# Optimization experiments

Measured on AMD Instinct MI355X. Metric: run time of the kernel, lower is better.

## Reference

```python
import jax, jax.numpy as jnp
import numpy as np

B, N, D, H, S = 32, 8192, 64, 128, 16
ITERS, TAU = 3, 0.1


def _ln(x, g, b):
    m = x.mean(-1, keepdims=True)
    v = ((x - m) ** 2).mean(-1, keepdims=True)
    return (x - m) / jnp.sqrt(v + 1e-5) * g + b


def setup_inputs() -> dict:
    key = jax.random.key(0)
    ks = jax.random.split(key, 20)
    nrm = lambda k, shp, s: jax.random.normal(k, shp, jnp.float32) * s
    return {
        'x': nrm(ks[0], (B, N, D), 1.0),
        'w1': nrm(ks[1], (D, H), D ** -0.5), 'b1': jnp.zeros((H,), jnp.float32),
        'ln1_g': jnp.ones((H,), jnp.float32), 'ln1_b': jnp.zeros((H,), jnp.float32),
        'w2': nrm(ks[2], (H, H), H ** -0.5), 'b2': jnp.zeros((H,), jnp.float32),
        'ln2_g': jnp.ones((H,), jnp.float32), 'ln2_b': jnp.zeros((H,), jnp.float32),
        'slot_mu': nrm(ks[3], (1, S, H), 0.1),
        'gru_wi': nrm(ks[4], (3 * H, H), H ** -0.5), 'gru_wh': nrm(ks[5], (3 * H, H), H ** -0.5),
        'gru_bi': jnp.zeros((3 * H,), jnp.float32), 'gru_bh': jnp.zeros((3 * H,), jnp.float32),
        'mlp_w1': nrm(ks[6], (H, H), H ** -0.5), 'mlp_b1': jnp.zeros((H,), jnp.float32),
        'mlp_w2': nrm(ks[7], (H, H), H ** -0.5), 'mlp_b2': jnp.zeros((H,), jnp.float32),
        'norm_g': jnp.ones((H,), jnp.float32), 'norm_b': jnp.zeros((H,), jnp.float32),
    }


def reference(x, w1, b1, ln1_g, ln1_b, w2, b2, ln2_g, ln2_b, slot_mu,
              gru_wi, gru_wh, gru_bi, gru_bh, mlp_w1, mlp_b1, mlp_w2, mlp_b2,
              norm_g, norm_b):
    Bb = x.shape[0]
    h = jax.nn.gelu(_ln(x @ w1 + b1, ln1_g, ln1_b), approximate=False)
    feats = _ln(h @ w2 + b2, ln2_g, ln2_b)              # [B,N,H]
    slots = jnp.broadcast_to(slot_mu, (Bb, S, H))
    f2 = jnp.sum(feats * feats, -1)                      # [B,N]
    attn = None
    for _ in range(ITERS):
        s2 = jnp.sum(slots * slots, -1)                  # [B,S]
        sf = jnp.einsum('bsh,bnh->bsn', slots, feats)
        dist_sq = -(s2[:, :, None] - 2.0 * sf + f2[:, None, :])  # -||s-f||^2
        attn = jax.nn.softmax(dist_sq / TAU, axis=1)     # softmax over slots
        w = attn / (attn.sum(2, keepdims=True) + 1e-8)
        updates = jnp.einsum('bsn,bnh->bsh', w, feats)
        # GRUCell (PyTorch gate order: r, z, n)
        gi = updates @ gru_wi.T + gru_bi
        gh = slots @ gru_wh.T + gru_bh
        ir, iz, inn = jnp.split(gi, 3, -1)
        hr, hz, hn = jnp.split(gh, 3, -1)
        r = jax.nn.sigmoid(ir + hr)
        z = jax.nn.sigmoid(iz + hz)
        n = jnp.tanh(inn + r * hn)
        new = (1.0 - z) * n + z * slots
        mlp_out = jax.nn.gelu(_ln(new, norm_g, norm_b) @ mlp_w1 + mlp_b1, approximate=False) @ mlp_w2 + mlp_b2
        slots = new + 0.2 * mlp_out
    return (slots, attn)
```

## Files before the change

kernel.cpp:

```cpp
#include <hip/hip_runtime.h>
#include <cstddef>
#include <cstdint>

#define B_ 32
#define N_ 8192
#define D_ 64
#define H_ 128
#define S_ 16
#define L2SCALE 14.426950408889634f

typedef unsigned short ushort_t;
typedef __attribute__((ext_vector_type(8))) short short8;
typedef __attribute__((ext_vector_type(4))) float f32x4;

#define NCHUNK 256
#define NBLK   (N_ / NCHUNK)
#define PSTRIDE 264

#define W1T_STR 72
#define W2T_STR 136

__device__ __forceinline__ float gelu_fast(float x){
    float z = fabsf(x) * 0.70710678118654752f;
    float t = 1.0f / fmaf(0.3275911f, z, 1.0f);
    float p = t*(0.254829592f + t*(-0.284496736f + t*(1.421413741f +
              t*(-1.453152027f + t*1.061405429f))));
    float e = __expf(-z*z);
    float erf_abs = 1.0f - p*e;
    float er = copysignf(erf_abs, x);
    return 0.5f * x * (1.0f + er);
}
__device__ __forceinline__ ushort_t f2bf(float f){
    unsigned u = __float_as_uint(f);
    unsigned r = (u + 0x7FFF + ((u >> 16) & 1)) >> 16;
    return (ushort_t)r;
}
__device__ __forceinline__ float bf2f(ushort_t h){
    return __uint_as_float(((unsigned)h) << 16);
}

__global__ __launch_bounds__(256) void gemm1_kernel(
    const float* __restrict__ x, const float* __restrict__ w1, const float* __restrict__ b1,
    const float* __restrict__ ln1g, const float* __restrict__ ln1b,
    ushort_t* __restrict__ h_hi, ushort_t* __restrict__ h_lo)
{
    __shared__ ushort_t w1t_hi[128*W1T_STR];
    __shared__ ushort_t w1t_lo[128*W1T_STR];

    const int tid  = threadIdx.x;
    const int w    = tid >> 6;
    const int l    = tid & 63;
    const int ln   = l & 15;
    const int quad = l >> 4;
    const size_t n0 = (size_t)blockIdx.x * 128;

    for (int i = tid; i < 8192; i += 256){
        int k = i >> 7, hc = i & 127;
        float v = w1[i];
        ushort_t hi = f2bf(v);
        w1t_hi[hc*W1T_STR + k] = hi;
        w1t_lo[hc*W1T_STR + k] = f2bf(v - bf2f(hi));
    }
    __syncthreads();

    for (int tt = 0; tt < 2; ++tt){
        const size_t row = n0 + (size_t)(w*2 + tt)*16 + ln;
        const float* xr = x + row*64;

        short8 bxh[2], bxl[2];
        #pragma unroll
        for (int kc = 0; kc < 2; ++kc){
            float4 a0 = *(const float4*)(xr + kc*32 + quad*8);
            float4 a1 = *(const float4*)(xr + kc*32 + quad*8 + 4);
            float v[8] = {a0.x,a0.y,a0.z,a0.w,a1.x,a1.y,a1.z,a1.w};
            #pragma unroll
            for (int j=0;j<8;++j){
                ushort_t hi = f2bf(v[j]);
                bxh[kc][j] = (short)hi;
                bxl[kc][j] = (short)f2bf(v[j] - bf2f(hi));
            }
        }

        f32x4 acc[8];
        #pragma unroll
        for (int ht=0;ht<8;++ht) acc[ht] = (f32x4){0.f,0.f,0.f,0.f};

        #pragma unroll
        for (int ht = 0; ht < 8; ++ht){
            #pragma unroll
            for (int kc = 0; kc < 2; ++kc){
                short8 ah = *(const short8*)&w1t_hi[(ht*16+ln)*W1T_STR + kc*32 + quad*8];
                short8 al = *(const short8*)&w1t_lo[(ht*16+ln)*W1T_STR + kc*32 + quad*8];
                acc[ht] = __builtin_amdgcn_mfma_f32_16x16x32_bf16(ah, bxh[kc], acc[ht], 0,0,0);
                acc[ht] = __builtin_amdgcn_mfma_f32_16x16x32_bf16(ah, bxl[kc], acc[ht], 0,0,0);
                acc[ht] = __builtin_amdgcn_mfma_f32_16x16x32_bf16(al, bxh[kc], acc[ht], 0,0,0);
            }
        }

        float vals[8][4];
        float s1 = 0.f, sq = 0.f;
        #pragma unroll
        for (int ht=0;ht<8;++ht){
            float bb[4]; *(float4*)bb = *(const float4*)(b1 + ht*16 + quad*4);
            #pragma unroll
            for (int r=0;r<4;++r){
                float v = acc[ht][r] + bb[r];
                vals[ht][r] = v; s1 += v; sq += v*v;
            }
        }
        s1 += __shfl_xor(s1,16); s1 += __shfl_xor(s1,32);
        sq += __shfl_xor(sq,16); sq += __shfl_xor(sq,32);
        float mean = s1 * (1.f/128.f);
        float var  = sq * (1.f/128.f) - mean*mean;
        float rs   = 1.f / sqrtf(var + 1e-5f);

        #pragma unroll
        for (int ht=0;ht<8;++ht){
            float gg[4]; *(float4*)gg = *(const float4*)(ln1g + ht*16 + quad*4);
            float be[4]; *(float4*)be = *(const float4*)(ln1b + ht*16 + quad*4);
            ushort_t oh[4], ol[4];
            #pragma unroll
            for (int r=0;r<4;++r){
                float t  = (vals[ht][r]-mean)*rs*gg[r] + be[r];
                float ge = gelu_fast(t);
                ushort_t hi = f2bf(ge);
                oh[r] = hi;
                ol[r] = f2bf(ge - bf2f(hi));
            }
            size_t off = row*128 + ht*16 + quad*4;
            *(ushort4*)(h_hi + off) = make_ushort4(oh[0],oh[1],oh[2],oh[3]);
            *(ushort4*)(h_lo + off) = make_ushort4(ol[0],ol[1],ol[2],ol[3]);
        }
    }
}

__global__ __launch_bounds__(256) void gemm2_kernel(
    ushort_t* __restrict__ buf_hi, ushort_t* __restrict__ buf_lo,
    const float* __restrict__ w2, const float* __restrict__ b2,
    const float* __restrict__ ln2g, const float* __restrict__ ln2b)
{
    __shared__ ushort_t w2t_hi[128*W2T_STR];
    __shared__ ushort_t w2t_lo[128*W2T_STR];

    const int tid  = threadIdx.x;
    const int w    = tid >> 6;
    const int l    = tid & 63;
    const int ln   = l & 15;
    const int quad = l >> 4;
    const size_t n0 = (size_t)blockIdx.x * 128;

    for (int i = tid; i < 16384; i += 256){
        int k = i >> 7, hc = i & 127;
        float v = w2[i];
        ushort_t hi = f2bf(v);
        w2t_hi[hc*W2T_STR + k] = hi;
        w2t_lo[hc*W2T_STR + k] = f2bf(v - bf2f(hi));
    }
    __syncthreads();

    size_t row[2];
    row[0] = n0 + (size_t)(w*2 + 0)*16 + ln;
    row[1] = n0 + (size_t)(w*2 + 1)*16 + ln;

    f32x4 acc[2][8];
    #pragma unroll
    for (int t2=0;t2<2;++t2)
        #pragma unroll
        for (int ht=0;ht<8;++ht) acc[t2][ht] = (f32x4){0.f,0.f,0.f,0.f};

    #pragma unroll
    for (int kc = 0; kc < 4; ++kc){
        short8 bh[2], bl[2];
        #pragma unroll
        for (int t2=0;t2<2;++t2){
            bh[t2] = *(const short8*)(buf_hi + row[t2]*128 + kc*32 + quad*8);
            bl[t2] = *(const short8*)(buf_lo + row[t2]*128 + kc*32 + quad*8);
        }
        #pragma unroll
        for (int ht = 0; ht < 8; ++ht){
            short8 ah = *(const short8*)&w2t_hi[(ht*16+ln)*W2T_STR + kc*32 + quad*8];
            short8 al = *(const short8*)&w2t_lo[(ht*16+ln)*W2T_STR + kc*32 + quad*8];
            #pragma unroll
            for (int t2=0;t2<2;++t2){
                acc[t2][ht] = __builtin_amdgcn_mfma_f32_16x16x32_bf16(ah, bh[t2], acc[t2][ht], 0,0,0);
                acc[t2][ht] = __builtin_amdgcn_mfma_f32_16x16x32_bf16(ah, bl[t2], acc[t2][ht], 0,0,0);
                acc[t2][ht] = __builtin_amdgcn_mfma_f32_16x16x32_bf16(al, bh[t2], acc[t2][ht], 0,0,0);
            }
        }
    }

    #pragma unroll
    for (int t2=0;t2<2;++t2){
        float vals[8][4];
        float s1 = 0.f, sq = 0.f;
        #pragma unroll
        for (int ht=0;ht<8;++ht){
            float bb[4]; *(float4*)bb = *(const float4*)(b2 + ht*16 + quad*4);
            #pragma unroll
            for (int r=0;r<4;++r){
                float v = acc[t2][ht][r] + bb[r];
                vals[ht][r] = v; s1 += v; sq += v*v;
            }
        }
        s1 += __shfl_xor(s1,16); s1 += __shfl_xor(s1,32);
        sq += __shfl_xor(sq,16); sq += __shfl_xor(sq,32);
        float mean = s1 * (1.f/128.f);
        float var  = sq * (1.f/128.f) - mean*mean;
        float rs   = 1.f / sqrtf(var + 1e-5f);
        #pragma unroll
        for (int ht=0;ht<8;++ht){
            float gg[4]; *(float4*)gg = *(const float4*)(ln2g + ht*16 + quad*4);
            float be[4]; *(float4*)be = *(const float4*)(ln2b + ht*16 + quad*4);
            ushort_t oh[4], ol[4];
            #pragma unroll
            for (int r=0;r<4;++r){
                float o = (vals[ht][r]-mean)*rs*gg[r] + be[r];
                ushort_t hi = f2bf(o);
                oh[r] = hi;
                ol[r] = f2bf(o - bf2f(hi));
            }
            size_t off = row[t2]*128 + ht*16 + quad*4;
            *(ushort4*)(buf_hi + off) = make_ushort4(oh[0],oh[1],oh[2],oh[3]);
            *(ushort4*)(buf_lo + off) = make_ushort4(ol[0],ol[1],ol[2],ol[3]);
        }
    }
}

__global__ void init_slots(const float* __restrict__ mu, float* __restrict__ slots){
    int i = blockIdx.x * 256 + threadIdx.x;
    slots[i] = mu[i & 2047];
}

__global__ __launch_bounds__(256, 3) void attn_kernel(
    const ushort_t* __restrict__ f_hi, const ushort_t* __restrict__ f_lo,
    const float* __restrict__ slots,
    float* __restrict__ pn, float* __restrict__ pd,
    float* __restrict__ attn_out, const int write_attn)
{
    __shared__ ushort_t P_hi[16*PSTRIDE];
    __shared__ ushort_t P_lo[16*PSTRIDE];
    __shared__ float    s2buf[16];
    __shared__ float    den_red[16];

    const int tid  = threadIdx.x;
    const int w    = tid >> 6;
    const int l    = tid & 63;
    const int ln   = l & 15;
    const int quad = l >> 4;
    const int b    = blockIdx.x >> 5;
    const int nc   = blockIdx.x & 31;
    const int n0   = nc * NCHUNK;

    if (tid < 16) den_red[tid] = 0.f;

    short8 sa_hi[4], sa_lo[4];
    float q2 = 0.f;
    {
        const float* sp = slots + ((size_t)(b*16 + ln))*128 + quad*8;
        #pragma unroll
        for (int ks=0; ks<4; ++ks){
            float4 v0 = *(const float4*)(sp + ks*32);
            float4 v1 = *(const float4*)(sp + ks*32 + 4);
            float v[8] = {v0.x,v0.y,v0.z,v0.w,v1.x,v1.y,v1.z,v1.w};
            #pragma unroll
            for (int j=0;j<8;++j){
                q2 += v[j]*v[j];
                ushort_t hi = f2bf(v[j]);
                float lo = v[j] - bf2f(hi);
                sa_hi[ks][j] = (short)hi;
                sa_lo[ks][j] = (short)f2bf(lo);
            }
        }
    }
    q2 += __shfl_xor(q2, 16);
    q2 += __shfl_xor(q2, 32);
    if (tid < 16) s2buf[tid] = q2;
    __syncthreads();

    float s2v[4];
    #pragma unroll
    for (int r=0;r<4;++r) s2v[r] = s2buf[quad*4 + r];

    float den_acc[4] = {0.f,0.f,0.f,0.f};
    const size_t fbase = (size_t)b*N_ + n0;

    #pragma unroll
    for (int t2=0; t2<4; ++t2){
        const int t  = w*4 + t2;
        const int nl = t*16 + ln;
        const size_t rowoff = (fbase + nl) * 128;

        short8 fh[4], fl[4];
        #pragma unroll
        for (int ks=0; ks<4; ++ks){
            fh[ks] = *(const short8*)(f_hi + rowoff + ks*32 + quad*8);
            fl[ks] = *(const short8*)(f_lo + rowoff + ks*32 + quad*8);
        }

        f32x4 d = {0.f,0.f,0.f,0.f};
        #pragma unroll
        for (int ks=0;ks<4;++ks) d = __builtin_amdgcn_mfma_f32_16x16x32_bf16(sa_hi[ks], fh[ks], d, 0,0,0);
        #pragma unroll
        for (int ks=0;ks<4;++ks) d = __builtin_amdgcn_mfma_f32_16x16x32_bf16(sa_hi[ks], fl[ks], d, 0,0,0);
        #pragma unroll
        for (int ks=0;ks<4;++ks) d = __builtin_amdgcn_mfma_f32_16x16x32_bf16(sa_lo[ks], fh[ks], d, 0,0,0);

        float L[4];
        #pragma unroll
        for (int r=0;r<4;++r) L[r] = (2.f*d[r] - s2v[r]) * L2SCALE;
        float mx = fmaxf(fmaxf(L[0],L[1]), fmaxf(L[2],L[3]));
        mx = fmaxf(mx, __shfl_xor(mx, 16));
        mx = fmaxf(mx, __shfl_xor(mx, 32));
        float e[4];
        float z = 0.f;
        #pragma unroll
        for (int r=0;r<4;++r){ e[r] = exp2f(L[r] - mx); z += e[r]; }
        z += __shfl_xor(z, 16);
        z += __shfl_xor(z, 32);
        float rz = 1.f / z;
        #pragma unroll
        for (int r=0;r<4;++r){
            float p = e[r] * rz;
            den_acc[r] += p;
            if (write_attn)
                attn_out[((size_t)(b*16 + quad*4 + r))*N_ + n0 + nl] = p;
            ushort_t ph = f2bf(p);
            float plr = p - bf2f(ph);
            P_hi[(quad*4+r)*PSTRIDE + nl] = ph;
            P_lo[(quad*4+r)*PSTRIDE + nl] = f2bf(plr);
        }
    }

    #pragma unroll
    for (int m=1; m<16; m<<=1){
        #pragma unroll
        for (int r=0;r<4;++r) den_acc[r] += __shfl_xor(den_acc[r], m);
    }
    if (ln == 0){
        #pragma unroll
        for (int r=0;r<4;++r) atomicAdd(&den_red[quad*4 + r], den_acc[r]);
    }
    __syncthreads();

    #pragma unroll
    for (int t2=0; t2<2; ++t2){
        const int ht = w*2 + t2;
        f32x4 dacc = {0.f,0.f,0.f,0.f};
        #pragma unroll 2
        for (int ks=0; ks<8; ++ks){
            short8 pah = *(const short8*)(&P_hi[ln*PSTRIDE + ks*32 + quad*8]);
            short8 pal = *(const short8*)(&P_lo[ln*PSTRIDE + ks*32 + quad*8]);
            short8 fbh, fbl;
            #pragma unroll
            for (int j=0;j<8;++j){
                size_t go = (fbase + (size_t)(ks*32 + quad*8 + j))*128 + ht*16 + ln;
                fbh[j] = (short)f_hi[go];
                fbl[j] = (short)f_lo[go];
            }
            dacc = __builtin_amdgcn_mfma_f32_16x16x32_bf16(pah, fbh, dacc, 0,0,0);
            dacc = __builtin_amdgcn_mfma_f32_16x16x32_bf16(pal, fbh, dacc, 0,0,0);
            dacc = __builtin_amdgcn_mfma_f32_16x16x32_bf16(pah, fbl, dacc, 0,0,0);
        }
        float* dst = pn + (size_t)blockIdx.x * 2048;
        #pragma unroll
        for (int r=0;r<4;++r)
            dst[(quad*4+r)*128 + ht*16 + ln] = dacc[r];
    }
    if (tid < 16) pd[blockIdx.x*16 + tid] = den_red[tid];
}

__global__ __launch_bounds__(256) void update_kernel(
    const float* __restrict__ pn, const float* __restrict__ pd,
    float* __restrict__ slots,
    const float* __restrict__ gwi, const float* __restrict__ gwh,
    const float* __restrict__ gbi, const float* __restrict__ gbh,
    const float* __restrict__ mw1, const float* __restrict__ mb1,
    const float* __restrict__ mw2, const float* __restrict__ mb2,
    const float* __restrict__ ng, const float* __restrict__ nbv,
    float* __restrict__ out_slots, const int write_out)
{
    __shared__ float us[512], sl[512], gbuf[3072], nbuf[512], lnb[512], qb[512];
    const int tid  = threadIdx.x;
    const int row0 = blockIdx.x * 4;

    for (int i = tid; i < 512; i += 256){
        int r = i >> 7, h = i & 127;
        int grow = row0 + r;
        int bb = grow >> 4, ss = grow & 15;
        float sum = 0.f, dv = 0.f;
        #pragma unroll 4
        for (int c = 0; c < NBLK; ++c)
            sum += pn[((size_t)(bb*NBLK + c))*2048 + ss*128 + h];
        #pragma unroll
        for (int c = 0; c < NBLK; ++c)
            dv += pd[(bb*NBLK + c)*16 + ss];
        us[i] = sum / (dv + 1e-8f);
        sl[i] = slots[(size_t)grow*128 + h];
    }
    __syncthreads();

    for (int idx = tid; idx < 3072; idx += 256){
        int which = idx >= 1536;
        int rem   = idx - which*1536;
        int r     = rem / 384;
        int o     = rem - r*384;
        const float* W   = which ? gwh : gwi;
        const float* bb  = which ? gbh : gbi;
        const float* src = (which ? sl : us) + r*128;
        float a = bb[o];
        const float4* Wr = (const float4*)(W + (size_t)o*128);
        #pragma unroll 8
        for (int k4=0;k4<32;++k4){
            float4 wv = Wr[k4];
            float4 sv = *(const float4*)(src + 4*k4);
            a += sv.x*wv.x + sv.y*wv.y + sv.z*wv.z + sv.w*wv.w;
        }
        gbuf[idx] = a;
    }
    __syncthreads();

    for (int i = tid; i < 512; i += 256){
        int r = i >> 7, h = i & 127;
        float ir  = gbuf[r*384 + h];
        float iz  = gbuf[r*384 + 128 + h];
        float in_ = gbuf[r*384 + 256 + h];
        float hr  = gbuf[1536 + r*384 + h];
        float hz  = gbuf[1536 + r*384 + 128 + h];
        float hn  = gbuf[1536 + r*384 + 256 + h];
        float rg = 1.f/(1.f + __expf(-(ir+hr)));
        float zg = 1.f/(1.f + __expf(-(iz+hz)));
        float nn = tanhf(in_ + rg*hn);
        nbuf[i] = (1.f - zg)*nn + zg*sl[i];
    }
    __syncthreads();

    {
        int wv = tid >> 6, ll = tid & 63;
        float v0 = nbuf[wv*128 + ll], v1 = nbuf[wv*128 + 64 + ll];
        float s1 = v0 + v1, sq = v0*v0 + v1*v1;
        #pragma unroll
        for (int m=1; m<64; m<<=1){ s1 += __shfl_xor(s1,m); sq += __shfl_xor(sq,m); }
        float mean = s1*(1.f/128.f), var = sq*(1.f/128.f) - mean*mean;
        float rs = 1.f/sqrtf(var + 1e-5f);
        lnb[wv*128 + ll]      = (v0-mean)*rs*ng[ll] + nbv[ll];
        lnb[wv*128 + 64 + ll] = (v1-mean)*rs*ng[64+ll] + nbv[64+ll];
    }
    __syncthreads();

    for (int i = tid; i < 512; i += 256){
        int r = i >> 7, o = i & 127;
        float a = mb1[o];
        const float* lr = lnb + r*128;
        #pragma unroll 8
        for (int k=0;k<128;++k) a += lr[k] * mw1[(size_t)k*128 + o];
        qb[i] = gelu_fast(a);
    }
    __syncthreads();

    for (int i = tid; i < 512; i += 256){
        int r = i >> 7, h = i & 127;
        float a = mb2[h];
        const float* qr = qb + r*128;
        #pragma unroll 8
        for (int k=0;k<128;++k) a += qr[k] * mw2[(size_t)k*128 + h];
        float ov = nbuf[i] + 0.2f*a;
        int grow = row0 + r;
        slots[(size_t)grow*128 + h] = ov;
        if (write_out) out_slots[(size_t)grow*128 + h] = ov;
    }
}

extern "C" void kernel_launch(void* const* d_in, const int* in_sizes, int n_in,
                              void* d_out, int out_size, void* d_ws, size_t ws_size,
                              hipStream_t stream)
{
    const float* x    = (const float*)d_in[0];
    const float* w1   = (const float*)d_in[1];
    const float* b1   = (const float*)d_in[2];
    const float* ln1g = (const float*)d_in[3];
    const float* ln1b = (const float*)d_in[4];
    const float* w2   = (const float*)d_in[5];
    const float* b2   = (const float*)d_in[6];
    const float* ln2g = (const float*)d_in[7];
    const float* ln2b = (const float*)d_in[8];
    const float* smu  = (const float*)d_in[9];
    const float* gwi  = (const float*)d_in[10];
    const float* gwh  = (const float*)d_in[11];
    const float* gbi  = (const float*)d_in[12];
    const float* gbh  = (const float*)d_in[13];
    const float* mw1  = (const float*)d_in[14];
    const float* mb1  = (const float*)d_in[15];
    const float* mw2  = (const float*)d_in[16];
    const float* mb2  = (const float*)d_in[17];
    const float* ng   = (const float*)d_in[18];
    const float* nbv  = (const float*)d_in[19];

    float* out_slots = (float*)d_out;
    float* out_attn  = (float*)d_out + (size_t)B_*S_*H_;

    ushort_t* buf_hi = (ushort_t*)d_ws;
    ushort_t* buf_lo = buf_hi + (size_t)B_*N_*H_;
    float* slots = (float*)(buf_lo + (size_t)B_*N_*H_);
    float* pn    = slots + B_*S_*H_;
    float* pd    = pn + (size_t)(B_*NBLK)*2048;

    gemm1_kernel<<<dim3(2048), dim3(256), 0, stream>>>(
        x, w1, b1, ln1g, ln1b, buf_hi, buf_lo);
    gemm2_kernel<<<dim3(2048), dim3(256), 0, stream>>>(
        buf_hi, buf_lo, w2, b2, ln2g, ln2b);
    init_slots<<<dim3(256), dim3(256), 0, stream>>>(smu, slots);

    for (int it = 0; it < 3; ++it){
        attn_kernel<<<dim3(B_*NBLK), dim3(256), 0, stream>>>(
            buf_hi, buf_lo, slots, pn, pd, out_attn, (it==2) ? 1 : 0);
        update_kernel<<<dim3(128), dim3(256), 0, stream>>>(
            pn, pd, slots, gwi, gwh, gbi, gbh, mw1, mb1, mw2, mb2, ng, nbv,
            out_slots, (it==2) ? 1 : 0);
    }
}
```

Before: 720.1 us.

## Fuse feature GEMMs, pre-split weights once, stage feats transposed in LDS for attention

Weight hi/lo bf16 splitting moves into a one-time prep kernel, and the two feature GEMMs are fused into one kernel. The hidden activations stay in LDS instead of round-tripping through global memory. The attention kernel now transposes the feature tile into shared memory while it computes logits. The weighted-sum MFMA then reads from LDS instead of doing strided scalar gathers from global memory, at the cost of more LDS use and lower occupancy, since the occupancy hint in the launch bounds is dropped.

Measured after the change: 618.1 us. 14.2% less time.

```diff
diff --git a/kernel.cpp b/kernel.cpp
--- a/kernel.cpp
+++ b/kernel.cpp
@@ -11,14 +11,14 @@
 
 typedef unsigned short ushort_t;
 typedef __attribute__((ext_vector_type(8))) short short8;
+typedef __attribute__((ext_vector_type(4))) short short4v;
 typedef __attribute__((ext_vector_type(4))) float f32x4;
 
 #define NCHUNK 256
 #define NBLK   (N_ / NCHUNK)
-#define PSTRIDE 264
-
-#define W1T_STR 72
-#define W2T_STR 136
+#define PSTR   140
+#define FTSTR  132
+#define HSTR   132
 
 __device__ __forceinline__ float gelu_fast(float x){
     float z = fabsf(x) * 0.70710678118654752f;
@@ -26,8 +26,7 @@
     float p = t*(0.254829592f + t*(-0.284496736f + t*(1.421413741f +
               t*(-1.453152027f + t*1.061405429f))));
     float e = __expf(-z*z);
-    float erf_abs = 1.0f - p*e;
-    float er = copysignf(erf_abs, x);
+    float er = copysignf(1.0f - p*e, x);
     return 0.5f * x * (1.0f + er);
 }
 __device__ __forceinline__ ushort_t f2bf(float f){
@@ -38,14 +37,43 @@
 __device__ __forceinline__ float bf2f(ushort_t h){
     return __uint_as_float(((unsigned)h) << 16);
 }
-
-__global__ __launch_bounds__(256) void gemm1_kernel(
-    const float* __restrict__ x, const float* __restrict__ w1, const float* __restrict__ b1,
-    const float* __restrict__ ln1g, const float* __restrict__ ln1b,
-    ushort_t* __restrict__ h_hi, ushort_t* __restrict__ h_lo)
+__device__ __forceinline__ short8 ld8x2(const ushort_t* p){
+    short4v a = *(const short4v*)p;
+    short4v b = *(const short4v*)(p + 4);
+    return __builtin_shufflevector(a, b, 0,1,2,3,4,5,6,7);
+}
+
+__global__ void prep_kernel(const float* __restrict__ w1, const float* __restrict__ w2,
+                            ushort_t* __restrict__ w1t_hi, ushort_t* __restrict__ w1t_lo,
+                            ushort_t* __restrict__ w2t_hi, ushort_t* __restrict__ w2t_lo)
 {
-    __shared__ ushort_t w1t_hi[128*W1T_STR];
-    __shared__ ushort_t w1t_lo[128*W1T_STR];
+    int i = blockIdx.x * 256 + threadIdx.x;
+    if (i < 8192){
+        int k = i >> 7, h = i & 127;
+        float v = w1[i];
+        ushort_t hi = f2bf(v);
+        w1t_hi[h*64 + k] = hi;
+        w1t_lo[h*64 + k] = f2bf(v - bf2f(hi));
+    }
+    {
+        int k = i >> 7, h = i & 127;
+        float v = w2[i];
+        ushort_t hi = f2bf(v);
+        w2t_hi[h*128 + k] = hi;
+        w2t_lo[h*128 + k] = f2bf(v - bf2f(hi));
+    }
+}
+
+__global__ __launch_bounds__(256) void feats_kernel(
+    const float* __restrict__ x,
+    const ushort_t* __restrict__ w1t_hi, const ushort_t* __restrict__ w1t_lo,
+    const ushort_t* __restrict__ w2t_hi, const ushort_t* __restrict__ w2t_lo,
+    const float* __restrict__ b1, const float* __restrict__ ln1g, const float* __restrict__ ln1b,
+    const float* __restrict__ b2, const float* __restrict__ ln2g, const float* __restrict__ ln2b,
+    ushort_t* __restrict__ f_hi, ushort_t* __restrict__ f_lo)
+{
+    __shared__ ushort_t hsh[128*HSTR];
+    __shared__ ushort_t hsl[128*HSTR];
 
     const int tid  = threadIdx.x;
     const int w    = tid >> 6;
@@ -54,17 +82,9 @@
     const int quad = l >> 4;
     const size_t n0 = (size_t)blockIdx.x * 128;
 
-    for (int i = tid; i < 8192; i += 256){
-        int k = i >> 7, hc = i & 127;
-        float v = w1[i];
-        ushort_t hi = f2bf(v);
-        w1t_hi[hc*W1T_STR + k] = hi;
-        w1t_lo[hc*W1T_STR + k] = f2bf(v - bf2f(hi));
-    }
-    __syncthreads();
-
-    for (int tt = 0; tt < 2; ++tt){
-        const size_t row = n0 + (size_t)(w*2 + tt)*16 + ln;
+    for (int t2 = 0; t2 < 2; ++t2){
+        const int rloc = (w*2 + t2)*16 + ln;
+        const size_t row = n0 + rloc;
         const float* xr = x + row*64;
 
         short8 bxh[2], bxl[2];
@@ -84,13 +104,12 @@
         f32x4 acc[8];
         #pragma unroll
         for (int ht=0;ht<8;++ht) acc[ht] = (f32x4){0.f,0.f,0.f,0.f};
-
         #pragma unroll
         for (int ht = 0; ht < 8; ++ht){
             #pragma unroll
             for (int kc = 0; kc < 2; ++kc){
-                short8 ah = *(const short8*)&w1t_hi[(ht*16+ln)*W1T_STR + kc*32 + quad*8];
-                short8 al = *(const short8*)&w1t_lo[(ht*16+ln)*W1T_STR + kc*32 + quad*8];
+                short8 ah = *(const short8*)&w1t_hi[(ht*16+ln)*64 + kc*32 + quad*8];
+                short8 al = *(const short8*)&w1t_lo[(ht*16+ln)*64 + kc*32 + quad*8];
                 acc[ht] = __builtin_amdgcn_mfma_f32_16x16x32_bf16(ah, bxh[kc], acc[ht], 0,0,0);
                 acc[ht] = __builtin_amdgcn_mfma_f32_16x16x32_bf16(ah, bxl[kc], acc[ht], 0,0,0);
                 acc[ht] = __builtin_amdgcn_mfma_f32_16x16x32_bf16(al, bxh[kc], acc[ht], 0,0,0);
@@ -118,79 +137,43 @@
         for (int ht=0;ht<8;++ht){
             float gg[4]; *(float4*)gg = *(const float4*)(ln1g + ht*16 + quad*4);
             float be[4]; *(float4*)be = *(const float4*)(ln1b + ht*16 + quad*4);
-            ushort_t oh[4], ol[4];
+            short4v oh, ol;
             #pragma unroll
             for (int r=0;r<4;++r){
                 float t  = (vals[ht][r]-mean)*rs*gg[r] + be[r];
                 float ge = gelu_fast(t);
                 ushort_t hi = f2bf(ge);
-                oh[r] = hi;
-                ol[r] = f2bf(ge - bf2f(hi));
-            }
-            size_t off = row*128 + ht*16 + quad*4;
-            *(ushort4*)(h_hi + off) = make_ushort4(oh[0],oh[1],oh[2],oh[3]);
-            *(ushort4*)(h_lo + off) = make_ushort4(ol[0],ol[1],ol[2],ol[3]);
-        }
-    }
-}
-
-__global__ __launch_bounds__(256) void gemm2_kernel(
-    ushort_t* __restrict__ buf_hi, ushort_t* __restrict__ buf_lo,
-    const float* __restrict__ w2, const float* __restrict__ b2,
-    const float* __restrict__ ln2g, const float* __restrict__ ln2b)
-{
-    __shared__ ushort_t w2t_hi[128*W2T_STR];
-    __shared__ ushort_t w2t_lo[128*W2T_STR];
-
-    const int tid  = threadIdx.x;
-    const int w    = tid >> 6;
-    const int l    = tid & 63;
-    const int ln   = l & 15;
-    const int quad = l >> 4;
-    const size_t n0 = (size_t)blockIdx.x * 128;
-
-    for (int i = tid; i < 16384; i += 256){
-        int k = i >> 7, hc = i & 127;
-        float v = w2[i];
-        ushort_t hi = f2bf(v);
-        w2t_hi[hc*W2T_STR + k] = hi;
-        w2t_lo[hc*W2T_STR + k] = f2bf(v - bf2f(hi));
-    }
-    __syncthreads();
-
-    size_t row[2];
-    row[0] = n0 + (size_t)(w*2 + 0)*16 + ln;
-    row[1] = n0 + (size_t)(w*2 + 1)*16 + ln;
-
-    f32x4 acc[2][8];
-    #pragma unroll
-    for (int t2=0;t2<2;++t2)
-        #pragma unroll
-        for (int ht=0;ht<8;++ht) acc[t2][ht] = (f32x4){0.f,0.f,0.f,0.f};
-
-    #pragma unroll
-    for (int kc = 0; kc < 4; ++kc){
-        short8 bh[2], bl[2];
-        #pragma unroll
-        for (int t2=0;t2<2;++t2){
-            bh[t2] = *(const short8*)(buf_hi + row[t2]*128 + kc*32 + quad*8);
-            bl[t2] = *(const short8*)(buf_lo + row[t2]*128 + kc*32 + quad*8);
-        }
-        #pragma unroll
-        for (int ht = 0; ht < 8; ++ht){
-            short8 ah = *(const short8*)&w2t_hi[(ht*16+ln)*W2T_STR + kc*32 + quad*8];
-            short8 al = *(const short8*)&w2t_lo[(ht*16+ln)*W2T_STR + kc*32 + quad*8];
-            #pragma unroll
-            for (int t2=0;t2<2;++t2){
-                acc[t2][ht] = __builtin_amdgcn_mfma_f32_16x16x32_bf16(ah, bh[t2], acc[t2][ht], 0,0,0);
-                acc[t2][ht] = __builtin_amdgcn_mfma_f32_16x16x32_bf16(ah, bl[t2], acc[t2][ht], 0,0,0);
-                acc[t2][ht] = __builtin_amdgcn_mfma_f32_16x16x32_bf16(al, bh[t2], acc[t2][ht], 0,0,0);
-            }
-        }
-    }
-
-    #pragma unroll
-    for (int t2=0;t2<2;++t2){
+                oh[r] = (short)hi;
+                ol[r] = (short)f2bf(ge - bf2f(hi));
+            }
+            *(short4v*)&hsh[rloc*HSTR + ht*16 + quad*4] = oh;
+            *(short4v*)&hsl[rloc*HSTR + ht*16 + quad*4] = ol;
+        }
+    }
+    __syncthreads();
+
+    for (int t2 = 0; t2 < 2; ++t2){
+        const int rloc = (w*2 + t2)*16 + ln;
+        const size_t row = n0 + rloc;
+
+        f32x4 acc2[8];
+        #pragma unroll
+        for (int ht=0;ht<8;++ht) acc2[ht] = (f32x4){0.f,0.f,0.f,0.f};
+
+        #pragma unroll
+        for (int kc = 0; kc < 4; ++kc){
+            short8 bh = ld8x2(&hsh[rloc*HSTR + kc*32 + quad*8]);
+            short8 bl = ld8x2(&hsl[rloc*HSTR + kc*32 + quad*8]);
+            #pragma unroll
+            for (int ht = 0; ht < 8; ++ht){
+                short8 ah = *(const short8*)&w2t_hi[(ht*16+ln)*128 + kc*32 + quad*8];
+                short8 al = *(const short8*)&w2t_lo[(ht*16+ln)*128 + kc*32 + quad*8];
+                acc2[ht] = __builtin_amdgcn_mfma_f32_16x16x32_bf16(ah, bh, acc2[ht], 0,0,0);
+                acc2[ht] = __builtin_amdgcn_mfma_f32_16x16x32_bf16(ah, bl, acc2[ht], 0,0,0);
+                acc2[ht] = __builtin_amdgcn_mfma_f32_16x16x32_bf16(al, bh, acc2[ht], 0,0,0);
+            }
+        }
+
         float vals[8][4];
         float s1 = 0.f, sq = 0.f;
         #pragma unroll
@@ -198,7 +181,7 @@
             float bb[4]; *(float4*)bb = *(const float4*)(b2 + ht*16 + quad*4);
             #pragma unroll
             for (int r=0;r<4;++r){
-                float v = acc[t2][ht][r] + bb[r];
+                float v = acc2[ht][r] + bb[r];
                 vals[ht][r] = v; s1 += v; sq += v*v;
             }
         }
@@ -207,6 +190,7 @@
         float mean = s1 * (1.f/128.f);
         float var  = sq * (1.f/128.f) - mean*mean;
         float rs   = 1.f / sqrtf(var + 1e-5f);
+
         #pragma unroll
         for (int ht=0;ht<8;++ht){
             float gg[4]; *(float4*)gg = *(const float4*)(ln2g + ht*16 + quad*4);
@@ -219,9 +203,9 @@
                 oh[r] = hi;
                 ol[r] = f2bf(o - bf2f(hi));
             }
-            size_t off = row[t2]*128 + ht*16 + quad*4;
-            *(ushort4*)(buf_hi + off) = make_ushort4(oh[0],oh[1],oh[2],oh[3]);
-            *(ushort4*)(buf_lo + off) = make_ushort4(ol[0],ol[1],ol[2],ol[3]);
+            size_t off = row*128 + ht*16 + quad*4;
+            *(ushort4*)(f_hi + off) = make_ushort4(oh[0],oh[1],oh[2],oh[3]);
+            *(ushort4*)(f_lo + off) = make_ushort4(ol[0],ol[1],ol[2],ol[3]);
         }
     }
 }
@@ -231,14 +215,16 @@
     slots[i] = mu[i & 2047];
 }
 
-__global__ __launch_bounds__(256, 3) void attn_kernel(
+__global__ __launch_bounds__(256) void attn_kernel(
     const ushort_t* __restrict__ f_hi, const ushort_t* __restrict__ f_lo,
     const float* __restrict__ slots,
     float* __restrict__ pn, float* __restrict__ pd,
     float* __restrict__ attn_out, const int write_attn)
 {
-    __shared__ ushort_t P_hi[16*PSTRIDE];
-    __shared__ ushort_t P_lo[16*PSTRIDE];
+    __shared__ ushort_t fTh[128*FTSTR];
+    __shared__ ushort_t fTl[128*FTSTR];
+    __shared__ ushort_t Ph[16*PSTR];
+    __shared__ ushort_t Pl[16*PSTR];
     __shared__ float    s2buf[16];
     __shared__ float    den_red[16];
 
@@ -266,9 +252,8 @@
             for (int j=0;j<8;++j){
                 q2 += v[j]*v[j];
                 ushort_t hi = f2bf(v[j]);
-                float lo = v[j] - bf2f(hi);
                 sa_hi[ks][j] = (short)hi;
-                sa_lo[ks][j] = (short)f2bf(lo);
+                sa_lo[ks][j] = (short)f2bf(v[j] - bf2f(hi));
             }
         }
     }
@@ -282,52 +267,91 @@
     for (int r=0;r<4;++r) s2v[r] = s2buf[quad*4 + r];
 
     float den_acc[4] = {0.f,0.f,0.f,0.f};
+    f32x4 dacc[2];
+    dacc[0] = (f32x4){0.f,0.f,0.f,0.f};
+    dacc[1] = (f32x4){0.f,0.f,0.f,0.f};
     const size_t fbase = (size_t)b*N_ + n0;
 
-    #pragma unroll
-    for (int t2=0; t2<4; ++t2){
-        const int t  = w*4 + t2;
-        const int nl = t*16 + ln;
-        const size_t rowoff = (fbase + nl) * 128;
-
-        short8 fh[4], fl[4];
-        #pragma unroll
-        for (int ks=0; ks<4; ++ks){
-            fh[ks] = *(const short8*)(f_hi + rowoff + ks*32 + quad*8);
-            fl[ks] = *(const short8*)(f_lo + rowoff + ks*32 + quad*8);
-        }
-
-        f32x4 d = {0.f,0.f,0.f,0.f};
-        #pragma unroll
-        for (int ks=0;ks<4;++ks) d = __builtin_amdgcn_mfma_f32_16x16x32_bf16(sa_hi[ks], fh[ks], d, 0,0,0);
-        #pragma unroll
-        for (int ks=0;ks<4;++ks) d = __builtin_amdgcn_mfma_f32_16x16x32_bf16(sa_hi[ks], fl[ks], d, 0,0,0);
-        #pragma unroll
-        for (int ks=0;ks<4;++ks) d = __builtin_amdgcn_mfma_f32_16x16x32_bf16(sa_lo[ks], fh[ks], d, 0,0,0);
-
-        float L[4];
-        #pragma unroll
-        for (int r=0;r<4;++r) L[r] = (2.f*d[r] - s2v[r]) * L2SCALE;
-        float mx = fmaxf(fmaxf(L[0],L[1]), fmaxf(L[2],L[3]));
-        mx = fmaxf(mx, __shfl_xor(mx, 16));
-        mx = fmaxf(mx, __shfl_xor(mx, 32));
-        float e[4];
-        float z = 0.f;
-        #pragma unroll
-        for (int r=0;r<4;++r){ e[r] = exp2f(L[r] - mx); z += e[r]; }
-        z += __shfl_xor(z, 16);
-        z += __shfl_xor(z, 32);
-        float rz = 1.f / z;
-        #pragma unroll
-        for (int r=0;r<4;++r){
-            float p = e[r] * rz;
-            den_acc[r] += p;
-            if (write_attn)
-                attn_out[((size_t)(b*16 + quad*4 + r))*N_ + n0 + nl] = p;
-            ushort_t ph = f2bf(p);
-            float plr = p - bf2f(ph);
-            P_hi[(quad*4+r)*PSTRIDE + nl] = ph;
-            P_lo[(quad*4+r)*PSTRIDE + nl] = f2bf(plr);
+    for (int hf = 0; hf < 2; ++hf){
+        if (hf) __syncthreads();
+
+        #pragma unroll
+        for (int t2=0; t2<2; ++t2){
+            const int nl = (w*2 + t2)*16 + ln;
+            const size_t rowoff = (fbase + hf*128 + nl) * 128;
+
+            short8 fh[4], fl[4];
+            #pragma unroll
+            for (int ks=0; ks<4; ++ks){
+                fh[ks] = *(const short8*)(f_hi + rowoff + ks*32 + quad*8);
+                fl[ks] = *(const short8*)(f_lo + rowoff + ks*32 + quad*8);
+            }
+            #pragma unroll
+            for (int ks=0; ks<4; ++ks){
+                #pragma unroll
+                for (int j=0;j<8;++j){
+                    fTh[(ks*32 + quad*8 + j)*FTSTR + nl] = (ushort_t)fh[ks][j];
+                    fTl[(ks*32 + quad*8 + j)*FTSTR + nl] = (ushort_t)fl[ks][j];
+                }
+            }
+
+            f32x4 d = {0.f,0.f,0.f,0.f};
+            #pragma unroll
+            for (int ks=0;ks<4;++ks) d = __builtin_amdgcn_mfma_f32_16x16x32_bf16(sa_hi[ks], fh[ks], d, 0,0,0);
+            #pragma unroll
+            for (int ks=0;ks<4;++ks) d = __builtin_amdgcn_mfma_f32_16x16x32_bf16(sa_hi[ks], fl[ks], d, 0,0,0);
+            #pragma unroll
+            for (int ks=0;ks<4;++ks) d = __builtin_amdgcn_mfma_f32_16x16x32_bf16(sa_lo[ks], fh[ks], d, 0,0,0);
+
+            float L[4];
+            #pragma unroll
+            for (int r=0;r<4;++r) L[r] = (2.f*d[r] - s2v[r]) * L2SCALE;
+            float mx = fmaxf(fmaxf(L[0],L[1]), fmaxf(L[2],L[3]));
+            mx = fmaxf(mx, __shfl_xor(mx, 16));
+            mx = fmaxf(mx, __shfl_xor(mx, 32));
+            float e[4];
+            float z = 0.f;
+            #pragma unroll
+            for (int r=0;r<4;++r){ e[r] = exp2f(L[r] - mx); z += e[r]; }
+            z += __shfl_xor(z, 16);
+            z += __shfl_xor(z, 32);
+            float rz = 1.f / z;
+            #pragma unroll
+            for (int r=0;r<4;++r){
+                float p = e[r] * rz;
+                den_acc[r] += p;
+                if (write_attn)
+                    attn_out[((size_t)(b*16 + quad*4 + r))*N_ + n0 + hf*128 + nl] = p;
+                ushort_t ph = f2bf(p);
+                Ph[(quad*4+r)*PSTR + nl] = ph;
+                Pl[(quad*4+r)*PSTR + nl] = f2bf(p - bf2f(ph));
+            }
+        }
+        __syncthreads();
+
+        #pragma unroll
+        for (int ht2=0; ht2<2; ++ht2){
+            const int ht = w*2 + ht2;
+            #pragma unroll
+            for (int ks=0; ks<4; ++ks){
+                short8 ah = ld8x2(&fTh[(ht*16 + ln)*FTSTR + ks*32 + quad*8]);
+                short8 al = ld8x2(&fTl[(ht*16 + ln)*FTSTR + ks*32 + quad*8]);
+                short8 bh = ld8x2(&Ph[ln*PSTR + ks*32 + quad*8]);
+                short8 bl = ld8x2(&Pl[ln*PSTR + ks*32 + quad*8]);
+                dacc[ht2] = __builtin_amdgcn_mfma_f32_16x16x32_bf16(ah, bh, dacc[ht2], 0,0,0);
+                dacc[ht2] = __builtin_amdgcn_mfma_f32_16x16x32_bf16(ah, bl, dacc[ht2], 0,0,0);
+                dacc[ht2] = __builtin_amdgcn_mfma_f32_16x16x32_bf16(al, bh, dacc[ht2], 0,0,0);
+            }
+        }
+    }
+
+    {
+        float* dst = pn + (size_t)blockIdx.x * 2048;
+        #pragma unroll
+        for (int ht2=0; ht2<2; ++ht2){
+            const int ht = w*2 + ht2;
+            *(float4*)(dst + ln*128 + ht*16 + quad*4) =
+                make_float4(dacc[ht2][0], dacc[ht2][1], dacc[ht2][2], dacc[ht2][3]);
         }
     }
 
@@ -341,31 +365,6 @@
         for (int r=0;r<4;++r) atomicAdd(&den_red[quad*4 + r], den_acc[r]);
     }
     __syncthreads();
-
-    #pragma unroll
-    for (int t2=0; t2<2; ++t2){
-        const int ht = w*2 + t2;
-        f32x4 dacc = {0.f,0.f,0.f,0.f};
-        #pragma unroll 2
-        for (int ks=0; ks<8; ++ks){
-            short8 pah = *(const short8*)(&P_hi[ln*PSTRIDE + ks*32 + quad*8]);
-            short8 pal = *(const short8*)(&P_lo[ln*PSTRIDE + ks*32 + quad*8]);
-            short8 fbh, fbl;
-            #pragma unroll
-            for (int j=0;j<8;++j){
-                size_t go = (fbase + (size_t)(ks*32 + quad*8 + j))*128 + ht*16 + ln;
-                fbh[j] = (short)f_hi[go];
-                fbl[j] = (short)f_lo[go];
-            }
-            dacc = __builtin_amdgcn_mfma_f32_16x16x32_bf16(pah, fbh, dacc, 0,0,0);
-            dacc = __builtin_amdgcn_mfma_f32_16x16x32_bf16(pal, fbh, dacc, 0,0,0);
-            dacc = __builtin_amdgcn_mfma_f32_16x16x32_bf16(pah, fbl, dacc, 0,0,0);
-        }
-        float* dst = pn + (size_t)blockIdx.x * 2048;
-        #pragma unroll
-        for (int r=0;r<4;++r)
-            dst[(quad*4+r)*128 + ht*16 + ln] = dacc[r];
-    }
     if (tid < 16) pd[blockIdx.x*16 + tid] = den_red[tid];
 }
 
@@ -498,21 +497,24 @@
     float* out_slots = (float*)d_out;
     float* out_attn  = (float*)d_out + (size_t)B_*S_*H_;
 
-    ushort_t* buf_hi = (ushort_t*)d_ws;
-    ushort_t* buf_lo = buf_hi + (size_t)B_*N_*H_;
-    float* slots = (float*)(buf_lo + (size_t)B_*N_*H_);
+    ushort_t* f_hi = (ushort_t*)d_ws;
+    ushort_t* f_lo = f_hi + (size_t)B_*N_*H_;
+    float* slots = (float*)(f_lo + (size_t)B_*N_*H_);
     float* pn    = slots + B_*S_*H_;
     float* pd    = pn + (size_t)(B_*NBLK)*2048;
-
-    gemm1_kernel<<<dim3(2048), dim3(256), 0, stream>>>(
-        x, w1, b1, ln1g, ln1b, buf_hi, buf_lo);
-    gemm2_kernel<<<dim3(2048), dim3(256), 0, stream>>>(
-        buf_hi, buf_lo, w2, b2, ln2g, ln2b);
+    ushort_t* w1t_hi = (ushort_t*)(pd + B_*NBLK*16);
+    ushort_t* w1t_lo = w1t_hi + 8192;
+    ushort_t* w2t_hi = w1t_lo + 8192;
+    ushort_t* w2t_lo = w2t_hi + 16384;
+
+    prep_kernel<<<dim3(64), dim3(256), 0, stream>>>(w1, w2, w1t_hi, w1t_lo, w2t_hi, w2t_lo);
+    feats_kernel<<<dim3(2048), dim3(256), 0, stream>>>(
+        x, w1t_hi, w1t_lo, w2t_hi, w2t_lo, b1, ln1g, ln1b, b2, ln2g, ln2b, f_hi, f_lo);
     init_slots<<<dim3(256), dim3(256), 0, stream>>>(smu, slots);
 
     for (int it = 0; it < 3; ++it){
         attn_kernel<<<dim3(B_*NBLK), dim3(256), 0, stream>>>(
-            buf_hi, buf_lo, slots, pn, pd, out_attn, (it==2) ? 1 : 0);
+            f_hi, f_lo, slots, pn, pd, out_attn, (it==2) ? 1 : 0);
         update_kernel<<<dim3(128), dim3(256), 0, stream>>>(
             pn, pd, slots, gwi, gwh, gbi, gbh, mw1, mb1, mw2, mb2, ng, nbv,
             out_slots, (it==2) ? 1 : 0);
```
